# Optimization experiments

Measured on AMD Instinct MI355X. Metric: run time of the kernel, lower is better.

Reference implementation:

```python
import jax, jax.numpy as jnp
import numpy as np

D_MODEL = 1024
NUM_HEADS = 16
D_HEAD = D_MODEL // NUM_HEADS
B, S = 4, 2048


def setup_inputs() -> dict:
    key = jax.random.key(0)
    ks = jax.random.split(key, 11)
    s = 1.0 / np.sqrt(D_MODEL)
    inp = {
        "query": jax.random.normal(ks[0], (B, S, D_MODEL), jnp.float32),
        "key": jax.random.normal(ks[1], (B, S, D_MODEL), jnp.float32),
        "value": jax.random.normal(ks[2], (B, S, D_MODEL), jnp.float32),
        "Wq": jax.random.uniform(ks[3], (D_MODEL, D_MODEL), jnp.float32, -s, s),
        "bq": jax.random.uniform(ks[4], (D_MODEL,), jnp.float32, -s, s),
        "Wk": jax.random.uniform(ks[5], (D_MODEL, D_MODEL), jnp.float32, -s, s),
        "bk": jax.random.uniform(ks[6], (D_MODEL,), jnp.float32, -s, s),
        "Wv": jax.random.uniform(ks[7], (D_MODEL, D_MODEL), jnp.float32, -s, s),
        "bv": jax.random.uniform(ks[8], (D_MODEL,), jnp.float32, -s, s),
        "Wo": jax.random.uniform(ks[9], (D_MODEL, D_MODEL), jnp.float32, -s, s),
        "bo": jax.random.uniform(ks[10], (D_MODEL,), jnp.float32, -s, s),
    }
    return inp


def reference(query, key, value, Wq, bq, Wk, bk, Wv, bv, Wo, bo):
    # Linear projections (torch Linear: x @ W.T + b)
    q = query @ Wq.T + bq  # [B,S,D]
    k = key @ Wk.T + bk
    v = value @ Wv.T + bv
    # split heads -> [B,H,S,Dh]
    def split(x):
        return x.reshape(B, S, NUM_HEADS, D_HEAD).transpose(0, 2, 1, 3)
    q, k, v = split(q), split(k), split(v)
    scale = 1.0 / np.sqrt(D_HEAD).astype(np.float32)
    scores = jnp.einsum('bhqd,bhkd->bhqk', q, k) * scale
    attn = jax.nn.softmax(scores, axis=-1)  # dropout is identity in eval
    ctx = jnp.einsum('bhqk,bhkd->bhqd', attn, v)
    ctx = ctx.transpose(0, 2, 1, 3).reshape(B, S, D_MODEL)
    return ctx @ Wo.T + bo
```

## Files before the change

kernel.cpp:

```cpp
#include <hip/hip_runtime.h>
#include <hip/hip_bf16.h>

typedef __bf16 bf16;
typedef bf16 bf16x8 __attribute__((ext_vector_type(8)));
typedef float f32x4 __attribute__((ext_vector_type(4)));
typedef float f32x16 __attribute__((ext_vector_type(16)));
typedef unsigned int u32x2 __attribute__((ext_vector_type(2)));
typedef unsigned int u32x4 __attribute__((ext_vector_type(4)));

#define B_  4
#define S_  2048
#define DM  1024
#define NH  16
#define DH  64

#define QSCALE 0.18033688011112042f


__device__ __forceinline__ void async_copy16(const void* g, void* lds) {
    __builtin_amdgcn_global_load_lds(
        (const __attribute__((address_space(1))) void*)g,
        (__attribute__((address_space(3))) void*)lds,
        16, 0, 0);
}

__device__ __forceinline__ bf16x8 read_frag(const char* lds, int row, int kbyte) {
    int off = row * 128 + (kbyte ^ ((row & 7) << 4));
    return *(const bf16x8*)(lds + off);
}

template<int ROWS>
__device__ __forceinline__ void stage_g2l(const bf16* g, int gs, char* lds) {
    int t = threadIdx.x;
#pragma unroll
    for (int i = 0; i < ROWS * 8 / 256; ++i) {
        int c = i * 256 + t;
        int r = c >> 3;
        int s = (c & 7) ^ (r & 7);
        async_copy16(g + r * gs + s * 8, lds + c * 16);
    }
}

__device__ __forceinline__ unsigned cvt_pk(float lo, float hi) {
    unsigned r;
    asm("v_cvt_pk_bf16_f32 %0, %1, %2" : "=v"(r) : "v"(lo), "v"(hi));
    return r;
}

__device__ __forceinline__ u32x2 pl32swap(unsigned a, unsigned b) {
    return __builtin_amdgcn_permlane32_swap(a, b, false, false);
}

__device__ __forceinline__ float xhalf_max(float v) {
    unsigned u = __builtin_bit_cast(unsigned, v);
    u32x2 r = pl32swap(u, u);
    return fmaxf(__builtin_bit_cast(float, r.x), __builtin_bit_cast(float, r.y));
}
__device__ __forceinline__ float xhalf_sum(float v) {
    unsigned u = __builtin_bit_cast(unsigned, v);
    u32x2 r = pl32swap(u, u);
    return __builtin_bit_cast(float, r.x) + __builtin_bit_cast(float, r.y);
}


__device__ __forceinline__ void cvt_body(const float* __restrict__ s, bf16* __restrict__ d, int n8) {
    for (int i = blockIdx.x * 256 + threadIdx.x; i < n8; i += gridDim.x * 256) {
        f32x4 v0 = *(const f32x4*)(s + (long)i * 8);
        f32x4 v1 = *(const f32x4*)(s + (long)i * 8 + 4);
        bf16x8 r;
#pragma unroll
        for (int j = 0; j < 4; ++j) { r[j] = (bf16)v0[j]; r[j + 4] = (bf16)v1[j]; }
        *(bf16x8*)(d + (long)i * 8) = r;
    }
}

__global__ __launch_bounds__(256) void cvt_x(
    const float* __restrict__ a, const float* __restrict__ b, const float* __restrict__ c,
    bf16* __restrict__ oa, bf16* __restrict__ ob, bf16* __restrict__ oc)
{
    int z = blockIdx.y;
    cvt_body(z == 0 ? a : z == 1 ? b : c, z == 0 ? oa : z == 1 ? ob : oc, B_ * S_ * DM / 8);
}

__global__ __launch_bounds__(256) void cvt_w(
    const float* __restrict__ a, const float* __restrict__ b,
    const float* __restrict__ c, const float* __restrict__ d,
    bf16* __restrict__ oa, bf16* __restrict__ ob, bf16* __restrict__ oc, bf16* __restrict__ od)
{
    int z = blockIdx.y;
    cvt_body(z == 0 ? a : z == 1 ? b : z == 2 ? c : d,
             z == 0 ? oa : z == 1 ? ob : z == 2 ? oc : od, DM * DM / 8);
}


__device__ __forceinline__ void gemm_main(
    const bf16* __restrict__ A, const bf16* __restrict__ Wt,
    char* As, char* Bs, int m0, int n0, int lane, int wm, int wn, f32x4 (&acc)[4][4])
{
#pragma unroll
    for (int i = 0; i < 4; ++i)
#pragma unroll
        for (int j = 0; j < 4; ++j) acc[i][j] = f32x4{0.f, 0.f, 0.f, 0.f};

    for (int k0 = 0; k0 < DM; k0 += 64) {
        __syncthreads();
        stage_g2l<128>(A + (long)m0 * DM + k0, DM, As);
        stage_g2l<128>(Wt + (long)n0 * DM + k0, DM, Bs);
        __syncthreads();
#pragma unroll
        for (int ks = 0; ks < 2; ++ks) {
            int kb = ks * 64 + (lane >> 4) * 16;
            bf16x8 af[4], bfr[4];
#pragma unroll
            for (int f = 0; f < 4; ++f) af[f]  = read_frag(As, wm + f * 16 + (lane & 15), kb);
#pragma unroll
            for (int f = 0; f < 4; ++f) bfr[f] = read_frag(Bs, wn + f * 16 + (lane & 15), kb);
#pragma unroll
            for (int mf = 0; mf < 4; ++mf)
#pragma unroll
                for (int nf = 0; nf < 4; ++nf)
                    acc[mf][nf] = __builtin_amdgcn_mfma_f32_16x16x32_bf16(
                        af[mf], bfr[nf], acc[mf][nf], 0, 0, 0);
        }
    }
}

__global__ __launch_bounds__(256) void qkv_gemm(
    const bf16* __restrict__ xq, const bf16* __restrict__ xk, const bf16* __restrict__ xv,
    const bf16* __restrict__ wq, const bf16* __restrict__ wk, const bf16* __restrict__ wv,
    const float* __restrict__ bq, const float* __restrict__ bk, const float* __restrict__ bv,
    bf16* __restrict__ qo, bf16* __restrict__ ko, bf16* __restrict__ vo)
{
    __shared__ alignas(128) char As[128 * 128];
    __shared__ alignas(128) char Bs[128 * 128];

    int z = blockIdx.z;
    const bf16* X     = (z == 0) ? xq : (z == 1) ? xk : xv;
    const bf16* W     = (z == 0) ? wq : (z == 1) ? wk : wv;
    const float* bias = (z == 0) ? bq : (z == 1) ? bk : bv;
    bf16* out         = (z == 0) ? qo : (z == 1) ? ko : vo;
    float scale       = (z == 0) ? QSCALE : 1.0f;
    bool  vt          = (z == 2);

    int m0 = blockIdx.y * 128, n0 = blockIdx.x * 128;
    int lane = threadIdx.x & 63, wid = threadIdx.x >> 6;
    int wm = (wid >> 1) * 64, wn = (wid & 1) * 64;

    f32x4 acc[4][4];
    gemm_main(X, W, As, Bs, m0, n0, lane, wm, wn, acc);

#pragma unroll
    for (int nf = 0; nf < 4; ++nf) {
        int j = n0 + wn + nf * 16 + (lane & 15);
        float bj = bias[j];
        int h = j >> 6, dh = j & 63;
#pragma unroll
        for (int mf = 0; mf < 4; ++mf) {
#pragma unroll
            for (int r = 0; r < 4; ++r) {
                int i = m0 + wm + mf * 16 + (lane >> 4) * 4 + r;
                float v = (acc[mf][nf][r] + bj) * scale;
                int b = i >> 11, s = i & 2047;
                long addr = vt ? ((long)((b * NH + h) * DH + dh)) * S_ + s
                               : ((long)((b * NH + h) * S_ + s)) * DH + dh;
                out[addr] = (bf16)v;
            }
        }
    }
}

__global__ __launch_bounds__(256) void out_gemm(
    const bf16* __restrict__ ctxb, const bf16* __restrict__ wo, const float* __restrict__ bo,
    float* __restrict__ out)
{
    __shared__ alignas(128) char As[128 * 128];
    __shared__ alignas(128) char Bs[128 * 128];

    int m0 = blockIdx.y * 128, n0 = blockIdx.x * 128;
    int lane = threadIdx.x & 63, wid = threadIdx.x >> 6;
    int wm = (wid >> 1) * 64, wn = (wid & 1) * 64;

    f32x4 acc[4][4];
    gemm_main(ctxb, wo, As, Bs, m0, n0, lane, wm, wn, acc);

#pragma unroll
    for (int nf = 0; nf < 4; ++nf) {
        int j = n0 + wn + nf * 16 + (lane & 15);
        float bj = bo[j];
#pragma unroll
        for (int mf = 0; mf < 4; ++mf)
#pragma unroll
            for (int r = 0; r < 4; ++r) {
                int i = m0 + wm + mf * 16 + (lane >> 4) * 4 + r;
                out[(long)i * DM + j] = acc[mf][nf][r] + bj;
            }
    }
}

__global__ __launch_bounds__(256) void attn_fwd(
    const bf16* __restrict__ qb, const bf16* __restrict__ kb, const bf16* __restrict__ vtb,
    bf16* __restrict__ ctx)
{
    __shared__ alignas(128) char Ks[2][64 * 128];
    __shared__ alignas(128) char Vs[2][64 * 128];

    int qt = blockIdx.x, bh = blockIdx.y;
    int lane = threadIdx.x & 63, wid = threadIdx.x >> 6;
    int ln = lane & 31, h = lane >> 5;
    int q0w = qt * 128 + wid * 32;

    const bf16* qg = qb + (long)bh * S_ * DH;
    const bf16* kg = kb + (long)bh * S_ * DH;
    const bf16* vg = vtb + (long)bh * DH * S_;

    bf16x8 qf[4];
#pragma unroll
    for (int s = 0; s < 4; ++s)
        qf[s] = *(const bf16x8*)(qg + (long)(q0w + ln) * DH + s * 16 + h * 8);

    f32x16 o[2];
#pragma unroll
    for (int t = 0; t < 2; ++t)
#pragma unroll
        for (int r = 0; r < 16; ++r) o[t][r] = 0.f;
    float mr = -1e30f, lr = 0.f;

    stage_g2l<64>(kg, DH, Ks[0]);
    stage_g2l<64>(vg, S_, Vs[0]);
    __syncthreads();

    int cur = 0;
    for (int kt2 = 0; kt2 < S_ / 64; ++kt2) {
        if (kt2 + 1 < S_ / 64) {
            stage_g2l<64>(kg + (long)(kt2 + 1) * 64 * DH, DH, Ks[cur ^ 1]);
            stage_g2l<64>(vg + (kt2 + 1) * 64, S_, Vs[cur ^ 1]);
        }

        f32x16 acc[2];
#pragma unroll
        for (int t = 0; t < 2; ++t)
#pragma unroll
            for (int r = 0; r < 16; ++r) acc[t][r] = 0.f;
#pragma unroll
        for (int t = 0; t < 2; ++t)
#pragma unroll
            for (int s = 0; s < 4; ++s) {
                bf16x8 ka = read_frag(Ks[cur], 32 * t + ln, 32 * s + 16 * h);
                acc[t] = __builtin_amdgcn_mfma_f32_32x32x16_bf16(ka, qf[s], acc[t], 0, 0, 0);
            }

        float mt = acc[0][0];
#pragma unroll
        for (int r = 1; r < 16; ++r) mt = fmaxf(mt, acc[0][r]);
#pragma unroll
        for (int r = 0; r < 16; ++r) mt = fmaxf(mt, acc[1][r]);
        mt = xhalf_max(mt);
        float mn = fmaxf(mr, mt);
        float so = __builtin_amdgcn_exp2f(mr - mn);
        float rs = 0.f;
#pragma unroll
        for (int t = 0; t < 2; ++t)
#pragma unroll
            for (int r = 0; r < 16; ++r) {
                float p = __builtin_amdgcn_exp2f(acc[t][r] - mn);
                acc[t][r] = p;
                rs += p;
            }
        rs = xhalf_sum(rs);
        lr = lr * so + rs;
        mr = mn;
#pragma unroll
        for (int t = 0; t < 2; ++t)
#pragma unroll
            for (int r = 0; r < 16; ++r) o[t][r] *= so;

        unsigned pf[4][4];
#pragma unroll
        for (int t = 0; t < 2; ++t)
#pragma unroll
            for (int hf = 0; hf < 2; ++hf) {
                int rb = 8 * hf;
                unsigned a0 = cvt_pk(acc[t][rb + 0], acc[t][rb + 1]);
                unsigned s0 = cvt_pk(acc[t][rb + 4], acc[t][rb + 5]);
                unsigned a1 = cvt_pk(acc[t][rb + 2], acc[t][rb + 3]);
                unsigned s1 = cvt_pk(acc[t][rb + 6], acc[t][rb + 7]);
                u32x2 r0 = pl32swap(a0, s0);
                u32x2 r1 = pl32swap(a1, s1);
                int kt = 2 * t + hf;
                pf[kt][0] = r0.x; pf[kt][2] = r0.y;
                pf[kt][1] = r1.x; pf[kt][3] = r1.y;
            }

#pragma unroll
        for (int dt = 0; dt < 2; ++dt)
#pragma unroll
            for (int kt = 0; kt < 4; ++kt) {
                bf16x8 va = read_frag(Vs[cur], 32 * dt + ln, 32 * kt + 16 * h);
                bf16x8 pb = __builtin_bit_cast(bf16x8,
                    u32x4{pf[kt][0], pf[kt][1], pf[kt][2], pf[kt][3]});
                o[dt] = __builtin_amdgcn_mfma_f32_32x32x16_bf16(va, pb, o[dt], 0, 0, 0);
            }

        __syncthreads();
        cur ^= 1;
    }

    int b = bh >> 4, head = bh & 15;
    float inv = 1.0f / lr;
    int s = q0w + ln;
    bf16* base = ctx + ((long)(b * S_ + s)) * DM + head * DH;
#pragma unroll
    for (int dt = 0; dt < 2; ++dt)
#pragma unroll
        for (int c = 0; c < 4; ++c) {
            int d0 = 32 * dt + 8 * c + 4 * h;
            u32x2 st;
            st.x = cvt_pk(o[dt][4 * c + 0] * inv, o[dt][4 * c + 1] * inv);
            st.y = cvt_pk(o[dt][4 * c + 2] * inv, o[dt][4 * c + 3] * inv);
            *(u32x2*)(base + d0) = st;
        }
}

extern "C" void kernel_launch(void* const* d_in, const int* in_sizes, int n_in,
                              void* d_out, int out_size, void* d_ws, size_t ws_size,
                              hipStream_t stream) {
    const float* query = (const float*)d_in[0];
    const float* key   = (const float*)d_in[1];
    const float* value = (const float*)d_in[2];
    const float* Wq = (const float*)d_in[3];
    const float* bq = (const float*)d_in[4];
    const float* Wk = (const float*)d_in[5];
    const float* bk = (const float*)d_in[6];
    const float* Wv = (const float*)d_in[7];
    const float* bv = (const float*)d_in[8];
    const float* Wo = (const float*)d_in[9];
    const float* bo = (const float*)d_in[10];
    float* out = (float*)d_out;

    char* ws = (char*)d_ws;
    const long MB = 1ll << 20;
    bf16* qb   = (bf16*)(ws + 0 * MB);
    bf16* kb   = (bf16*)(ws + 16 * MB);
    bf16* vtb  = (bf16*)(ws + 32 * MB);
    bf16* xqb  = (bf16*)(ws + 48 * MB);
    bf16* xkb  = (bf16*)(ws + 64 * MB);
    bf16* xvb  = (bf16*)(ws + 80 * MB);
    bf16* wqb  = (bf16*)(ws + 96 * MB);
    bf16* wkb  = (bf16*)(ws + 98 * MB);
    bf16* wvb  = (bf16*)(ws + 100 * MB);
    bf16* wob  = (bf16*)(ws + 102 * MB);
    bf16* ctxb = xqb;

    dim3 blk(256);
    cvt_x<<<dim3(2048, 3), blk, 0, stream>>>(query, key, value, xqb, xkb, xvb);
    cvt_w<<<dim3(512, 4), blk, 0, stream>>>(Wq, Wk, Wv, Wo, wqb, wkb, wvb, wob);
    qkv_gemm<<<dim3(8, 64, 3), blk, 0, stream>>>(xqb, xkb, xvb, wqb, wkb, wvb,
                                                 bq, bk, bv, qb, kb, vtb);
    attn_fwd<<<dim3(16, 64), blk, 0, stream>>>(qb, kb, vtb, ctxb);
    out_gemm<<<dim3(8, 64), blk, 0, stream>>>(ctxb, wob, bo, out);
}
```

Baseline: 258.7 us.

## Defer softmax rescale, reorder QK before prefetch, add setprio and XCD-aware block mapping

```diff
diff --git a/kernel.cpp b/kernel.cpp
--- a/kernel.cpp
+++ b/kernel.cpp
@@ -15,6 +15,7 @@
 #define DH  64
 
 #define QSCALE 0.18033688011112042f
+#define DEFER_THR 8.0f
 
 
 __device__ __forceinline__ void async_copy16(const void* g, void* lds) {
@@ -204,7 +205,10 @@
     __shared__ alignas(128) char Ks[2][64 * 128];
     __shared__ alignas(128) char Vs[2][64 * 128];
 
-    int qt = blockIdx.x, bh = blockIdx.y;
+    int bid = blockIdx.x;
+    int xcd = bid & 7, rest = bid >> 3;
+    int qt = rest & 15, bh = xcd + 8 * (rest >> 4);
+
     int lane = threadIdx.x & 63, wid = threadIdx.x >> 6;
     int ln = lane & 31, h = lane >> 5;
     int q0w = qt * 128 + wid * 32;
@@ -231,48 +235,63 @@
 
     int cur = 0;
     for (int kt2 = 0; kt2 < S_ / 64; ++kt2) {
+        f32x16 acc[2];
+#pragma unroll
+        for (int t = 0; t < 2; ++t)
+#pragma unroll
+            for (int r = 0; r < 16; ++r) acc[t][r] = 0.f;
+        __builtin_amdgcn_s_setprio(1);
+#pragma unroll
+        for (int t = 0; t < 2; ++t)
+#pragma unroll
+            for (int s = 0; s < 4; ++s) {
+                bf16x8 ka = read_frag(Ks[cur], 32 * t + ln, 32 * s + 16 * h);
+                acc[t] = __builtin_amdgcn_mfma_f32_32x32x16_bf16(ka, qf[s], acc[t], 0, 0, 0);
+            }
+        __builtin_amdgcn_s_setprio(0);
+
         if (kt2 + 1 < S_ / 64) {
             stage_g2l<64>(kg + (long)(kt2 + 1) * 64 * DH, DH, Ks[cur ^ 1]);
             stage_g2l<64>(vg + (kt2 + 1) * 64, S_, Vs[cur ^ 1]);
         }
 
-        f32x16 acc[2];
+        float m4[8];
+#pragma unroll
+        for (int g = 0; g < 8; ++g) {
+            int t = g >> 2, rb = (g & 3) * 4;
+            m4[g] = fmaxf(fmaxf(acc[t][rb], acc[t][rb + 1]),
+                          fmaxf(acc[t][rb + 2], acc[t][rb + 3]));
+        }
+        float mt = fmaxf(fmaxf(fmaxf(m4[0], m4[1]), fmaxf(m4[2], m4[3])),
+                         fmaxf(fmaxf(m4[4], m4[5]), fmaxf(m4[6], m4[7])));
+        mt = xhalf_max(mt);
+
+        if (__any(mt - mr > DEFER_THR)) {
+            float mn = fmaxf(mr, mt);
+            float so = __builtin_amdgcn_exp2f(mr - mn);
+#pragma unroll
+            for (int t = 0; t < 2; ++t)
+#pragma unroll
+                for (int r = 0; r < 16; ++r) o[t][r] *= so;
+            lr *= so;
+            mr = mn;
+        }
+
 #pragma unroll
         for (int t = 0; t < 2; ++t)
 #pragma unroll
-            for (int r = 0; r < 16; ++r) acc[t][r] = 0.f;
-#pragma unroll
-        for (int t = 0; t < 2; ++t)
-#pragma unroll
-            for (int s = 0; s < 4; ++s) {
-                bf16x8 ka = read_frag(Ks[cur], 32 * t + ln, 32 * s + 16 * h);
-                acc[t] = __builtin_amdgcn_mfma_f32_32x32x16_bf16(ka, qf[s], acc[t], 0, 0, 0);
-            }
-
-        float mt = acc[0][0];
-#pragma unroll
-        for (int r = 1; r < 16; ++r) mt = fmaxf(mt, acc[0][r]);
-#pragma unroll
-        for (int r = 0; r < 16; ++r) mt = fmaxf(mt, acc[1][r]);
-        mt = xhalf_max(mt);
-        float mn = fmaxf(mr, mt);
-        float so = __builtin_amdgcn_exp2f(mr - mn);
-        float rs = 0.f;
-#pragma unroll
-        for (int t = 0; t < 2; ++t)
-#pragma unroll
-            for (int r = 0; r < 16; ++r) {
-                float p = __builtin_amdgcn_exp2f(acc[t][r] - mn);
-                acc[t][r] = p;
-                rs += p;
-            }
+            for (int r = 0; r < 16; ++r)
+                acc[t][r] = __builtin_amdgcn_exp2f(acc[t][r] - mr);
+
+        float s4[8];
+#pragma unroll
+        for (int g = 0; g < 8; ++g) {
+            int t = g >> 2, rb = (g & 3) * 4;
+            s4[g] = (acc[t][rb] + acc[t][rb + 1]) + (acc[t][rb + 2] + acc[t][rb + 3]);
+        }
+        float rs = ((s4[0] + s4[1]) + (s4[2] + s4[3])) + ((s4[4] + s4[5]) + (s4[6] + s4[7]));
         rs = xhalf_sum(rs);
-        lr = lr * so + rs;
-        mr = mn;
-#pragma unroll
-        for (int t = 0; t < 2; ++t)
-#pragma unroll
-            for (int r = 0; r < 16; ++r) o[t][r] *= so;
+        lr += rs;
 
         unsigned pf[4][4];
 #pragma unroll
@@ -291,6 +310,7 @@
                 pf[kt][1] = r1.x; pf[kt][3] = r1.y;
             }
 
+        __builtin_amdgcn_s_setprio(1);
 #pragma unroll
         for (int dt = 0; dt < 2; ++dt)
 #pragma unroll
@@ -300,6 +320,7 @@
                     u32x4{pf[kt][0], pf[kt][1], pf[kt][2], pf[kt][3]});
                 o[dt] = __builtin_amdgcn_mfma_f32_32x32x16_bf16(va, pb, o[dt], 0, 0, 0);
             }
+        __builtin_amdgcn_s_setprio(0);
 
         __syncthreads();
         cur ^= 1;
@@ -356,6 +377,6 @@
     cvt_w<<<dim3(512, 4), blk, 0, stream>>>(Wq, Wk, Wv, Wo, wqb, wkb, wvb, wob);
     qkv_gemm<<<dim3(8, 64, 3), blk, 0, stream>>>(xqb, xkb, xvb, wqb, wkb, wvb,
                                                  bq, bk, bv, qb, kb, vtb);
-    attn_fwd<<<dim3(16, 64), blk, 0, stream>>>(qb, kb, vtb, ctxb);
+    attn_fwd<<<dim3(1024), blk, 0, stream>>>(qb, kb, vtb, ctxb);
     out_gemm<<<dim3(8, 64), blk, 0, stream>>>(ctxb, wob, bo, out);
 }
```

After: 250.1 us. -3.4%, faster.
